# Optimization experiments

Hardware: AMD Instinct MI355X
Metric: run time of the kernel (lower is better)

## Reference

```python
import math
import jax, jax.numpy as jnp
import numpy as np

D = 1152      # vision_dim
P = 14        # patch
IMG = 896     # image_size
CIN = 3       # vision_channels
L = 2         # vision_blocks
MLP = 4304    # vision_mlp_hidden
EPS = 1e-6
B = 1
N = (IMG // P) ** 2  # 4096 tokens


def _ln(x, w, b):
    m = jnp.mean(x, axis=-1, keepdims=True)
    v = jnp.mean(jnp.square(x - m), axis=-1, keepdims=True)
    return (x - m) * jax.lax.rsqrt(v + EPS) * w + b


def setup_inputs() -> dict:
    key = jax.random.key(0)
    ks = jax.random.split(key, 20)
    s = 0.02
    inp = {
        "img": jax.random.normal(ks[0], (B, CIN, IMG, IMG), jnp.float32),
        "patch_w": jax.random.normal(ks[1], (D, CIN, P, P), jnp.float32) * s,
        "patch_b": jnp.zeros((D,), jnp.float32),
        "pos": jax.random.normal(ks[2], (D, N), jnp.float32) * s,
        # per-block params stacked along leading L axis (torch Linear: [out, in])
        "ln1_w": jnp.ones((L, D), jnp.float32),
        "ln1_b": jnp.zeros((L, D), jnp.float32),
        "qkv_w": jax.random.normal(ks[3], (L, 3 * D, D), jnp.float32) * s,
        "qkv_b": jnp.zeros((L, 3 * D), jnp.float32),
        "proj_w": jax.random.normal(ks[4], (L, D, D), jnp.float32) * s,
        "proj_b": jnp.zeros((L, D), jnp.float32),
        "ln2_w": jnp.ones((L, D), jnp.float32),
        "ln2_b": jnp.zeros((L, D), jnp.float32),
        "fc1_w": jax.random.normal(ks[5], (L, MLP, D), jnp.float32) * s,
        "fc1_b": jnp.zeros((L, MLP), jnp.float32),
        "fc2_w": jax.random.normal(ks[6], (L, D, MLP), jnp.float32) * s,
        "fc2_b": jnp.zeros((L, D), jnp.float32),
        "post_w": jnp.ones((D,), jnp.float32),
        "post_b": jnp.zeros((D,), jnp.float32),
    }
    return inp


def reference(img, patch_w, patch_b, pos, ln1_w, ln1_b, qkv_w, qkv_b,
              proj_w, proj_b, ln2_w, ln2_b, fc1_w, fc1_b, fc2_w, fc2_b,
              post_w, post_b):
    # conv patch embed (kernel=stride=P, valid padding)
    x = jax.lax.conv_general_dilated(
        img, patch_w, window_strides=(P, P), padding="VALID",
        dimension_numbers=("NCHW", "OIHW", "NCHW"))
    x = x + patch_b[None, :, None, None]
    x = x.reshape(B, D, N).transpose(0, 2, 1)          # [B, N, D]
    x = x + pos.T[None, :, :]

    scale = 1.0 / math.sqrt(D)

    def blk(x, p):
        l1w, l1b, qw, qb, pw, pb, l2w, l2b, f1w, f1b, f2w, f2b = p
        h = _ln(x, l1w, l1b)
        qkv = jnp.einsum("bnd,ed->bne", h, qw) + qb     # [B, N, 3D]
        q, k, v = jnp.split(qkv, 3, axis=-1)            # single-head, full D
        attn = jax.nn.softmax(jnp.einsum("bnd,bmd->bnm", q, k) * scale, axis=-1)
        y = jnp.einsum("bnm,bmd->bnd", attn, v)
        x = x + jnp.einsum("bnd,ed->bne", y, pw) + pb
        h = _ln(x, l2w, l2b)
        h = jax.nn.gelu(jnp.einsum("bnd,md->bnm", h, f1w) + f1b, approximate=False)
        x = x + jnp.einsum("bnm,dm->bnd", h, f2w) + f2b
        return x, None

    x, _ = jax.lax.scan(blk, x, (ln1_w, ln1_b, qkv_w, qkv_b, proj_w, proj_b,
                                 ln2_w, ln2_b, fc1_w, fc1_b, fc2_w, fc2_b))
    return _ln(x, post_w, post_b)
```

## Files before the change

### kernel.cpp

```cpp
#include <hip/hip_runtime.h>

#define NT 4096
#define DD 1152
#define D3 3456
#define MLP_R 4304
#define MLP_P 4352
#define KP 640

typedef unsigned short u16;
typedef short v8s __attribute__((ext_vector_type(8)));
typedef float v4f __attribute__((ext_vector_type(4)));

__device__ __forceinline__ u16 f2b(float f) {
    unsigned int u = __builtin_bit_cast(unsigned int, f);
    u += 0x7fffu + ((u >> 16) & 1u);
    return (u16)(u >> 16);
}
__device__ __forceinline__ float b2f(u16 s) {
    unsigned int u = ((unsigned int)s) << 16;
    return __builtin_bit_cast(float, u);
}

__device__ __forceinline__ void async16(const void* g, void* l) {
    __builtin_amdgcn_global_load_lds(
        (const __attribute__((address_space(1))) void*)g,
        (__attribute__((address_space(3))) void*)l, 16, 0, 0);
}

__device__ __forceinline__ unsigned lds_off(const void* p) {
    return (unsigned)(size_t)(const __attribute__((address_space(3))) void*)p;
}
__device__ __forceinline__ v8s ldsr(unsigned byte_off) {
    v8s r;
    asm volatile("ds_read_b128 %0, %1" : "=v"(r) : "v"(byte_off));
    return r;
}

__device__ __forceinline__ float gelu_f(float t) {
    float u = t * (0.7978845608028654f + 0.03567740814183026f * t * t);
    return t / (1.0f + __expf(-2.0f * u));
}

template<int EPI>
__global__ __launch_bounds__(512, 2)
void gemm8p(const u16* __restrict__ A, const u16* __restrict__ B, int ld,
            int Kdim, const float* __restrict__ bias,
            u16* __restrict__ outb, int ldc, int NNT)
{
    __shared__ __align__(128) union { u16 kl[2][32768]; u16 ep[8][8192]; } sm;
    const int tid  = threadIdx.x, lane = tid & 63, wave = tid >> 6;
    const int wr   = wave >> 2, wc = wave & 3;
    const int fr   = lane & 15, kqh = lane >> 4;

    const int nwg  = gridDim.x;
    const int bidx = (int)blockIdx.x;
    const int wg   = (bidx & 7) * (nwg >> 3) + (bidx >> 3);
    const int mt   = wg / NNT, nt = wg % NNT;
    const int bm0  = mt * 256, bn0 = nt * 256;

    const int c    = tid;
    const int s_lr = (c >> 7) * 16 + ((c >> 2) & 15);
    const int s_lc = ((((c >> 6) & 1) * 4) + ((c & 3) ^ (((c >> 5) & 1) << 1))) * 8;
    const size_t s_off = (size_t)s_lr * ld + s_lc;
    const unsigned koff2 = (unsigned)(fr * 64 + ((kqh * 16) ^ ((fr & 8) << 2)));

    u16* kb = sm.kl[0];
    const unsigned lbase = lds_off(kb);

    auto stage = [&](int bi, int reg, const u16* gRowBase) {
        u16* lb = kb + bi * 32768 + reg * 4096;
        async16(gRowBase + s_off, lb + tid * 8);
        async16(gRowBase + s_off + (size_t)64 * ld, lb + (512 + tid) * 8);
    };
    auto srcA = [&](int h, int t) { return A + (size_t)(bm0 + h * 128) * ld + t * 64; };
    auto srcB = [&](int h, int t) { return B + (size_t)(bn0 + h * 128) * ld + t * 64; };

    v4f acc[8][4];
    const v4f vzero = {0.f, 0.f, 0.f, 0.f};
#pragma unroll
    for (int i = 0; i < 8; ++i)
#pragma unroll
        for (int j = 0; j < 4; ++j) acc[i][j] = vzero;

    const int NKT = Kdim >> 6;

    stage(0, 4, srcB(0, 0));
    stage(0, 6, srcB(1, 0));
    stage(0, 0, srcA(0, 0));
    stage(0, 2, srcA(1, 0));
    if (NKT > 1) {
        stage(1, 4, srcB(0, 1));
        stage(1, 6, srcB(1, 1));
        asm volatile("s_waitcnt vmcnt(4)" ::: "memory");
    } else {
        asm volatile("s_waitcnt vmcnt(0)" ::: "memory");
    }
    __builtin_amdgcn_s_barrier();

    v8s a[8], b0f[4], b1f[4];
    for (int t = 0; t < NKT; ++t) {
        const int bi = t & 1;
        const unsigned AB = lbase + bi * 65536 + wr * 16384;
        const unsigned BB = lbase + bi * 65536 + 32768 + (wc >> 1) * 16384;
        const unsigned bs = (wc & 1) * 8192;

#pragma unroll
        for (int mi = 0; mi < 4; ++mi)
#pragma unroll
            for (int ks = 0; ks < 2; ++ks)
                a[mi * 2 + ks] = ldsr(AB + (mi * 2 + ks) * 1024 + koff2);
#pragma unroll
        for (int nj = 0; nj < 2; ++nj)
#pragma unroll
            for (int ks = 0; ks < 2; ++ks)
                b0f[nj * 2 + ks] = ldsr(BB + bs + (nj * 2 + ks) * 1024 + koff2);
        if (t + 1 < NKT) stage(bi ^ 1, 0, srcA(0, t + 1));
        __builtin_amdgcn_s_barrier();
        asm volatile("s_waitcnt lgkmcnt(0)" ::: "memory");
        __builtin_amdgcn_sched_barrier(0);
        __builtin_amdgcn_s_setprio(1);
#pragma unroll
        for (int mi = 0; mi < 4; ++mi)
#pragma unroll
            for (int nj = 0; nj < 2; ++nj)
#pragma unroll
                for (int ks = 0; ks < 2; ++ks)
                    acc[mi][nj] = __builtin_amdgcn_mfma_f32_16x16x32_bf16(
                        a[mi * 2 + ks], b0f[nj * 2 + ks], acc[mi][nj], 0, 0, 0);
        __builtin_amdgcn_s_setprio(0);
        __builtin_amdgcn_s_barrier();

#pragma unroll
        for (int nj = 0; nj < 2; ++nj)
#pragma unroll
            for (int ks = 0; ks < 2; ++ks)
                b1f[nj * 2 + ks] = ldsr(BB + bs + (4 + nj * 2 + ks) * 1024 + koff2);
        if (t + 1 < NKT) stage(bi ^ 1, 2, srcA(1, t + 1));
        __builtin_amdgcn_s_barrier();
        asm volatile("s_waitcnt lgkmcnt(0)" ::: "memory");
        __builtin_amdgcn_sched_barrier(0);
        __builtin_amdgcn_s_setprio(1);
#pragma unroll
        for (int mi = 0; mi < 4; ++mi)
#pragma unroll
            for (int nj = 0; nj < 2; ++nj)
#pragma unroll
                for (int ks = 0; ks < 2; ++ks)
                    acc[mi][2 + nj] = __builtin_amdgcn_mfma_f32_16x16x32_bf16(
                        a[mi * 2 + ks], b1f[nj * 2 + ks], acc[mi][2 + nj], 0, 0, 0);
        __builtin_amdgcn_s_setprio(0);
        __builtin_amdgcn_s_barrier();

#pragma unroll
        for (int mi = 0; mi < 4; ++mi)
#pragma unroll
            for (int ks = 0; ks < 2; ++ks)
                a[mi * 2 + ks] = ldsr(AB + (8 + mi * 2 + ks) * 1024 + koff2);
        if (t + 2 < NKT) stage(bi, 4, srcB(0, t + 2));
        __builtin_amdgcn_s_barrier();
        asm volatile("s_waitcnt lgkmcnt(0)" ::: "memory");
        __builtin_amdgcn_sched_barrier(0);
        __builtin_amdgcn_s_setprio(1);
#pragma unroll
        for (int mi = 0; mi < 4; ++mi)
#pragma unroll
            for (int nj = 0; nj < 2; ++nj)
#pragma unroll
                for (int ks = 0; ks < 2; ++ks)
                    acc[4 + mi][2 + nj] = __builtin_amdgcn_mfma_f32_16x16x32_bf16(
                        a[mi * 2 + ks], b1f[nj * 2 + ks], acc[4 + mi][2 + nj], 0, 0, 0);
        __builtin_amdgcn_s_setprio(0);
        __builtin_amdgcn_s_barrier();

        if (t + 2 < NKT) stage(bi, 6, srcB(1, t + 2));
        __builtin_amdgcn_s_barrier();
        __builtin_amdgcn_s_setprio(1);
#pragma unroll
        for (int mi = 0; mi < 4; ++mi)
#pragma unroll
            for (int nj = 0; nj < 2; ++nj)
#pragma unroll
                for (int ks = 0; ks < 2; ++ks)
                    acc[4 + mi][nj] = __builtin_amdgcn_mfma_f32_16x16x32_bf16(
                        a[mi * 2 + ks], b0f[nj * 2 + ks], acc[4 + mi][nj], 0, 0, 0);
        __builtin_amdgcn_s_setprio(0);
        asm volatile("s_waitcnt vmcnt(4)" ::: "memory");
        __builtin_amdgcn_s_barrier();
    }

    asm volatile("s_waitcnt vmcnt(0)" ::: "memory");
    __builtin_amdgcn_s_barrier();
    u16* ew = sm.ep[wave];
    float bcol[4];
    if constexpr (EPI >= 1) {
#pragma unroll
        for (int nj = 0; nj < 4; ++nj)
            bcol[nj] = bias[bn0 + wc * 64 + nj * 16 + fr];
    }
#pragma unroll
    for (int mi = 0; mi < 8; ++mi)
#pragma unroll
        for (int nj = 0; nj < 4; ++nj)
#pragma unroll
            for (int r = 0; r < 4; ++r) {
                int row = mi * 16 + kqh * 4 + r;
                int ec  = nj * 16 + fr;
                float t = acc[mi][nj][r];
                if constexpr (EPI >= 1) t += bcol[nj];
                if constexpr (EPI == 2) t = gelu_f(t);
                ew[row * 64 + (ec ^ (((row >> 2) & 3) << 4))] = f2b(t);
            }
    __syncthreads();
#pragma unroll
    for (int p = 0; p < 16; ++p) {
        int row = p * 8 + (lane >> 3);
        int key = (row >> 2) & 3;
        v8s ch = *(const v8s*)(ew + row * 64 + (((lane & 7) * 8) ^ (key << 4)));
        size_t gm = (size_t)(bm0 + wr * 128 + row);
        int gc = bn0 + wc * 64 + (lane & 7) * 8;
        *(uint4*)(outb + gm * ldc + gc) = __builtin_bit_cast(uint4, ch);
    }
}

template<int EPI, int MT, int DBUF = 0>
__global__ __launch_bounds__(256)
void gemm_bt(const u16* __restrict__ A, int lda,
             const u16* __restrict__ B, int ldb, int Kdim,
             const float* __restrict__ bias, const float* __restrict__ aux,
             float* __restrict__ outf, u16* __restrict__ outb, int ldc,
             u16* __restrict__ vt, int NX)
{
    constexpr int JT = (MT == 128) ? 4 : 2;
    constexpr int AR = MT * 8 / 256;
    constexpr int NB = DBUF ? 2 : 1;

    __shared__ union SM {
        struct { u16 a[NB * MT * 64]; u16 b[NB * 128 * 64]; } st;
        float sc[4][64][17];
    } sm;

    const int b    = blockIdx.x;
    const int MY   = (gridDim.x >> 3) / NX;
    const int q    = b >> 3;
    const int m0   = ((b & 7) * MY + q % MY) * MT;
    const int n0   = (q / MY) * 128;

    const int tid  = threadIdx.x;
    const int lane = tid & 63;
    const int wave = tid >> 6;
    const int wm   = (MT == 128) ? (wave & 1) * 64 : 0;
    const int wn   = (MT == 128) ? (wave >> 1) * 64 : wave * 32;
    const int fr   = lane & 15;
    const int kqh  = lane >> 4;
    const int swz  = fr & 7;

    v4f acc[4][JT];
    const v4f vzero = {0.f, 0.f, 0.f, 0.f};
#pragma unroll
    for (int i = 0; i < 4; ++i)
#pragma unroll
        for (int j = 0; j < JT; ++j) acc[i][j] = vzero;

    auto stage = [&](u16* As, u16* Bs, int kt) {
#pragma unroll
        for (int r = 0; r < AR; ++r) {
            int c = r * 256 + tid;
            int row = c >> 3;
            int kc = (c & 7) ^ (row & 7);
            async16(A + (size_t)(m0 + row) * lda + kt + kc * 8, As + c * 8);
        }
#pragma unroll
        for (int r = 0; r < 4; ++r) {
            int c = r * 256 + tid;
            int row = c >> 3;
            int kc = (c & 7) ^ (row & 7);
            async16(B + (size_t)(n0 + row) * ldb + kt + kc * 8, Bs + c * 8);
        }
    };

    auto compute = [&](const u16* As, const u16* Bs) {
#pragma unroll
        for (int ks = 0; ks < 2; ++ks) {
            const int kq = ks * 4 + kqh;
            const int kp = (kq ^ swz) * 8;
            v8s af[4], bf[JT];
#pragma unroll
            for (int i = 0; i < 4; ++i)
                af[i] = *(const v8s*)(As + (wm + i * 16 + fr) * 64 + kp);
#pragma unroll
            for (int j = 0; j < JT; ++j)
                bf[j] = *(const v8s*)(Bs + (wn + j * 16 + fr) * 64 + kp);
#pragma unroll
            for (int i = 0; i < 4; ++i)
#pragma unroll
                for (int j = 0; j < JT; ++j)
                    acc[i][j] = __builtin_amdgcn_mfma_f32_16x16x32_bf16(
                        af[i], bf[j], acc[i][j], 0, 0, 0);
        }
    };

    if constexpr (DBUF) {
        stage(sm.st.a, sm.st.b, 0);
        int cur = 0;
        for (int kt = 0; kt < Kdim; kt += 64) {
            __syncthreads();
            const int nxt = cur ^ 1;
            if (kt + 64 < Kdim)
                stage(sm.st.a + nxt * (MT * 64), sm.st.b + nxt * (128 * 64), kt + 64);
            compute(sm.st.a + cur * (MT * 64), sm.st.b + cur * (128 * 64));
            cur = nxt;
        }
    } else {
        for (int kt = 0; kt < Kdim; kt += 64) {
            stage(sm.st.a, sm.st.b, kt);
            __syncthreads();
            compute(sm.st.a, sm.st.b);
            __syncthreads();
        }
    }

    const int cn = lane & 15;
    const int cm = (lane >> 4) * 4;
    float (*S)[17] = sm.sc[wave];
    const int gm = m0 + wm + lane;
#pragma unroll
    for (int jp = 0; jp < JT; ++jp) {
        __syncthreads();
#pragma unroll
        for (int i = 0; i < 4; ++i)
#pragma unroll
            for (int r = 0; r < 4; ++r)
                S[i * 16 + cm + r][cn] = acc[i][jp][r];
        __syncthreads();
        const int gn0 = n0 + wn + jp * 16;
        float v[16];
#pragma unroll
        for (int c = 0; c < 16; ++c) v[c] = S[lane][c];
        if constexpr (EPI <= 2) {
            union { u16 us[16]; uint4 q4[2]; } o;
#pragma unroll
            for (int c = 0; c < 16; ++c) {
                float t = v[c];
                if constexpr (EPI >= 1) t += bias[gn0 + c];
                if constexpr (EPI == 2) t = gelu_f(t);
                o.us[c] = f2b(t);
            }
            uint4* dst = (uint4*)(outb + (size_t)gm * ldc + gn0);
            dst[0] = o.q4[0];
            dst[1] = o.q4[1];
            if constexpr (EPI == 1) {
                if (vt != nullptr && gn0 >= 2304) {
#pragma unroll
                    for (int c = 0; c < 16; ++c)
                        vt[(size_t)(gn0 + c - 2304) * NT + gm] = o.us[c];
                }
            }
        } else if constexpr (EPI == 3) {
            float* dst = outf + (size_t)gm * ldc + gn0;
            const float* ax = aux + (size_t)gm * ldc + gn0;
#pragma unroll
            for (int c = 0; c < 4; ++c) {
                float4 a4 = ((const float4*)ax)[c];
                float4 r4;
                r4.x = a4.x + v[4 * c + 0] + bias[gn0 + 4 * c + 0];
                r4.y = a4.y + v[4 * c + 1] + bias[gn0 + 4 * c + 1];
                r4.z = a4.z + v[4 * c + 2] + bias[gn0 + 4 * c + 2];
                r4.w = a4.w + v[4 * c + 3] + bias[gn0 + 4 * c + 3];
                ((float4*)dst)[c] = r4;
            }
        } else {
            float* dst = outf + (size_t)gm * ldc + gn0;
#pragma unroll
            for (int c = 0; c < 4; ++c) {
                float4 r4;
                r4.x = v[4 * c + 0] + bias[gn0 + 4 * c + 0] + aux[(size_t)(gn0 + 4 * c + 0) * NT + gm];
                r4.y = v[4 * c + 1] + bias[gn0 + 4 * c + 1] + aux[(size_t)(gn0 + 4 * c + 1) * NT + gm];
                r4.z = v[4 * c + 2] + bias[gn0 + 4 * c + 2] + aux[(size_t)(gn0 + 4 * c + 2) * NT + gm];
                r4.w = v[4 * c + 3] + bias[gn0 + 4 * c + 3] + aux[(size_t)(gn0 + 4 * c + 3) * NT + gm];
                ((float4*)dst)[c] = r4;
            }
        }
    }
}

template<int OUTF>
__global__ __launch_bounds__(384)
void ln_kernel(const float* __restrict__ x, const float* __restrict__ w,
               const float* __restrict__ b, void* __restrict__ out)
{
    const int n = blockIdx.x;
    const int t = threadIdx.x;
    const float* row = x + (size_t)n * DD;
    float v0 = row[t], v1 = row[t + 384], v2 = row[t + 768];
    float s  = v0 + v1 + v2;
    float ss = v0 * v0 + v1 * v1 + v2 * v2;
#pragma unroll
    for (int o = 32; o > 0; o >>= 1) {
        s  += __shfl_down(s, o);
        ss += __shfl_down(ss, o);
    }
    __shared__ float ps[6], pss[6], mh[2];
    if ((t & 63) == 0) { ps[t >> 6] = s; pss[t >> 6] = ss; }
    __syncthreads();
    if (t == 0) {
        float S = 0.f, SS = 0.f;
        for (int i = 0; i < 6; ++i) { S += ps[i]; SS += pss[i]; }
        float m = S / (float)DD;
        float var = SS / (float)DD - m * m;
        mh[0] = m;
        mh[1] = rsqrtf(var + 1e-6f);
    }
    __syncthreads();
    const float m = mh[0], rs = mh[1];
#pragma unroll
    for (int j = 0; j < 3; ++j) {
        int c = t + j * 384;
        float y = (row[c] - m) * rs * w[c] + b[c];
        if constexpr (OUTF) ((float*)out)[(size_t)n * DD + c] = y;
        else                ((u16*)out)[(size_t)n * DD + c]   = f2b(y);
    }
}

__global__ __launch_bounds__(256)
void softmax_kernel(u16* __restrict__ s)
{
    const float SC = 0.029462782549439484f;
    const int row = blockIdx.x;
    const int t = threadIdx.x;
    u16* p = s + (size_t)row * NT + t * 16;
    uint4 u0 = *(const uint4*)p;
    uint4 u1 = *(const uint4*)(p + 8);
    float v[16];
    unsigned int w[8] = {u0.x, u0.y, u0.z, u0.w, u1.x, u1.y, u1.z, u1.w};
#pragma unroll
    for (int i = 0; i < 8; ++i) {
        v[2 * i]     = b2f((u16)(w[i] & 0xffffu)) * SC;
        v[2 * i + 1] = b2f((u16)(w[i] >> 16)) * SC;
    }
    float mx = -1e30f;
#pragma unroll
    for (int i = 0; i < 16; ++i) mx = fmaxf(mx, v[i]);
#pragma unroll
    for (int o = 32; o > 0; o >>= 1) mx = fmaxf(mx, __shfl_down(mx, o));
    __shared__ float red[4];
    __shared__ float bc;
    if ((t & 63) == 0) red[t >> 6] = mx;
    __syncthreads();
    if (t == 0) bc = fmaxf(fmaxf(red[0], red[1]), fmaxf(red[2], red[3]));
    __syncthreads();
    const float M = bc;
    float sum = 0.f;
#pragma unroll
    for (int i = 0; i < 16; ++i) { v[i] = __expf(v[i] - M); sum += v[i]; }
#pragma unroll
    for (int o = 32; o > 0; o >>= 1) sum += __shfl_down(sum, o);
    __syncthreads();
    if ((t & 63) == 0) red[t >> 6] = sum;
    __syncthreads();
    if (t == 0) bc = red[0] + red[1] + red[2] + red[3];
    __syncthreads();
    const float inv = 1.0f / bc;
    union { u16 us[8]; uint4 u4; } o0, o1;
#pragma unroll
    for (int i = 0; i < 8; ++i) o0.us[i] = f2b(v[i] * inv);
#pragma unroll
    for (int i = 0; i < 8; ++i) o1.us[i] = f2b(v[8 + i] * inv);
    *(uint4*)p = o0.u4;
    *(uint4*)(p + 8) = o1.u4;
}

__global__ __launch_bounds__(256)
void im2col_kernel(const float* __restrict__ img, u16* __restrict__ a)
{
    const int k = blockIdx.x * 256 + threadIdx.x;
    const int n = blockIdx.y;
    if (k >= KP) return;
    float v = 0.f;
    if (k < 588) {
        int cin = k / 196;
        int rr = k - cin * 196;
        int py = rr / 14;
        int px = rr - py * 14;
        int gy = (n >> 6) * 14 + py;
        int gx = (n & 63) * 14 + px;
        v = img[(size_t)cin * 896 * 896 + (size_t)gy * 896 + gx];
    }
    a[(size_t)n * KP + k] = f2b(v);
}

constexpr int CV_S0 = 2 * D3 * DD / 4;
constexpr int CV_S1 = CV_S0 + 2 * DD * DD / 4;
constexpr int CV_S2 = CV_S1 + 2 * MLP_P * DD / 4;
constexpr int CV_S3 = CV_S2 + 2 * DD * MLP_P / 4;
constexpr int CV_S4 = CV_S3 + DD * KP / 4;
constexpr int CV_S5 = CV_S4 + 2 * MLP_P / 4;
constexpr int CV_BLOCKS = (CV_S5 + 255) / 256;

__device__ __forceinline__ void store_bf4(u16* p, float4 f) {
    union { u16 s[4]; uint2 d; } o;
    o.s[0] = f2b(f.x); o.s[1] = f2b(f.y); o.s[2] = f2b(f.z); o.s[3] = f2b(f.w);
    *(uint2*)p = o.d;
}

__global__ __launch_bounds__(256)
void convert_all(const float* __restrict__ qkv_w, const float* __restrict__ proj_w,
                 const float* __restrict__ fc1_w, const float* __restrict__ fc2_w,
                 const float* __restrict__ patch_w, const float* __restrict__ fc1_b,
                 u16* __restrict__ w_qkv, u16* __restrict__ w_proj,
                 u16* __restrict__ w_fc1, u16* __restrict__ w_fc2,
                 u16* __restrict__ w_pat, float* __restrict__ fc1b_p)
{
    int v = blockIdx.x * 256 + threadIdx.x;
    if (v >= CV_S5) return;
    const float4 z4 = {0.f, 0.f, 0.f, 0.f};
    if (v < CV_S0) {
        store_bf4(w_qkv + (size_t)v * 4, ((const float4*)qkv_w)[v]);
    } else if (v < CV_S1) {
        int e = v - CV_S0;
        store_bf4(w_proj + (size_t)e * 4, ((const float4*)proj_w)[e]);
    } else if (v < CV_S2) {
        size_t e = (size_t)(v - CV_S1) * 4;
        int row = (int)(e / DD);
        int c = (int)(e % DD);
        int l = row / MLP_P, lr = row % MLP_P;
        float4 f = z4;
        if (lr < MLP_R)
            f = *(const float4*)(fc1_w + ((size_t)l * MLP_R + lr) * DD + c);
        store_bf4(w_fc1 + e, f);
    } else if (v < CV_S3) {
        size_t e = (size_t)(v - CV_S2) * 4;
        int row = (int)(e / MLP_P);
        int c = (int)(e % MLP_P);
        float4 f = z4;
        if (c < MLP_R)
            f = *(const float4*)(fc2_w + (size_t)row * MLP_R + c);
        store_bf4(w_fc2 + e, f);
    } else if (v < CV_S4) {
        size_t e = (size_t)(v - CV_S3) * 4;
        int row = (int)(e / KP);
        int c = (int)(e % KP);
        float4 f = z4;
        if (c < 588)
            f = *(const float4*)(patch_w + (size_t)row * 588 + c);
        store_bf4(w_pat + e, f);
    } else {
        size_t e = (size_t)(v - CV_S4) * 4;
        int l = (int)(e / MLP_P);
        int c = (int)(e % MLP_P);
        float4 f = z4;
        if (c < MLP_R)
            f = *(const float4*)(fc1_b + (size_t)l * MLP_R + c);
        *(float4*)(fc1b_p + e) = f;
    }
}

constexpr size_t OFF_X      = 0;
constexpr size_t OFF_HBF    = OFF_X      + (size_t)NT * DD * 4;
constexpr size_t OFF_TMP    = OFF_HBF    + (size_t)NT * DD * 2;
constexpr size_t OFF_QKV    = OFF_TMP    + (size_t)NT * MLP_P * 2;
constexpr size_t OFF_VT     = OFF_QKV    + (size_t)NT * D3 * 2;
constexpr size_t OFF_IM     = OFF_VT     + (size_t)DD * NT * 2;
constexpr size_t OFF_WQKV   = OFF_IM     + (size_t)NT * KP * 2;
constexpr size_t OFF_WPROJ  = OFF_WQKV   + (size_t)2 * D3 * DD * 2;
constexpr size_t OFF_WFC1   = OFF_WPROJ  + (size_t)2 * DD * DD * 2;
constexpr size_t OFF_WFC2   = OFF_WFC1   + (size_t)2 * MLP_P * DD * 2;
constexpr size_t OFF_WPATCH = OFF_WFC2   + (size_t)2 * DD * MLP_P * 2;
constexpr size_t OFF_FC1B   = OFF_WPATCH + (size_t)DD * KP * 2;

extern "C" void kernel_launch(void* const* d_in, const int* in_sizes, int n_in,
                              void* d_out, int out_size, void* d_ws, size_t ws_size,
                              hipStream_t stream)
{
    const float* img     = (const float*)d_in[0];
    const float* patch_w = (const float*)d_in[1];
    const float* patch_b = (const float*)d_in[2];
    const float* pos     = (const float*)d_in[3];
    const float* ln1_w   = (const float*)d_in[4];
    const float* ln1_b   = (const float*)d_in[5];
    const float* qkv_w   = (const float*)d_in[6];
    const float* qkv_b   = (const float*)d_in[7];
    const float* proj_w  = (const float*)d_in[8];
    const float* proj_b  = (const float*)d_in[9];
    const float* ln2_w   = (const float*)d_in[10];
    const float* ln2_b   = (const float*)d_in[11];
    const float* fc1_w   = (const float*)d_in[12];
    const float* fc1_b   = (const float*)d_in[13];
    const float* fc2_w   = (const float*)d_in[14];
    const float* fc2_b   = (const float*)d_in[15];
    const float* post_w  = (const float*)d_in[16];
    const float* post_b  = (const float*)d_in[17];

    char* ws = (char*)d_ws;
    float* x      = (float*)(ws + OFF_X);
    u16*  h_bf    = (u16*)(ws + OFF_HBF);
    u16*  tmp_bf  = (u16*)(ws + OFF_TMP);
    u16*  qkv_bf  = (u16*)(ws + OFF_QKV);
    u16*  vt      = (u16*)(ws + OFF_VT);
    u16*  a_im    = (u16*)(ws + OFF_IM);
    u16*  w_qkv   = (u16*)(ws + OFF_WQKV);
    u16*  w_proj  = (u16*)(ws + OFF_WPROJ);
    u16*  w_fc1   = (u16*)(ws + OFF_WFC1);
    u16*  w_fc2   = (u16*)(ws + OFF_WFC2);
    u16*  w_pat   = (u16*)(ws + OFF_WPATCH);
    float* fc1b_p = (float*)(ws + OFF_FC1B);

    convert_all<<<CV_BLOCKS, 256, 0, stream>>>(
        qkv_w, proj_w, fc1_w, fc2_w, patch_w, fc1_b,
        w_qkv, w_proj, w_fc1, w_fc2, w_pat, fc1b_p);
    im2col_kernel<<<dim3(3, NT), 256, 0, stream>>>(img, a_im);

    gemm_bt<4, 64, 1><<<9 * 64, 256, 0, stream>>>(
        a_im, KP, w_pat, KP, KP, patch_b, pos, x, nullptr, DD, nullptr, 9);

    for (int l = 0; l < 2; ++l) {
        ln_kernel<0><<<NT, 384, 0, stream>>>(x, ln1_w + l * DD, ln1_b + l * DD, h_bf);
        gemm_bt<1, 128><<<27 * 32, 256, 0, stream>>>(
            h_bf, DD, w_qkv + (size_t)l * D3 * DD, DD, DD,
            qkv_b + (size_t)l * D3, nullptr, nullptr, qkv_bf, D3, vt, 27);
        gemm8p<0><<<256, 512, 0, stream>>>(
            qkv_bf, qkv_bf + DD, D3, DD, nullptr, tmp_bf, NT, 16);
        softmax_kernel<<<NT, 256, 0, stream>>>(tmp_bf);
        gemm_bt<0, 64, 1><<<9 * 64, 256, 0, stream>>>(
            tmp_bf, NT, vt, NT, NT, nullptr, nullptr, nullptr, h_bf, DD, nullptr, 9);
        gemm_bt<3, 64, 1><<<9 * 64, 256, 0, stream>>>(
            h_bf, DD, w_proj + (size_t)l * DD * DD, DD, DD,
            proj_b + (size_t)l * DD, x, x, nullptr, DD, nullptr, 9);
        ln_kernel<0><<<NT, 384, 0, stream>>>(x, ln2_w + l * DD, ln2_b + l * DD, h_bf);
        gemm8p<2><<<272, 512, 0, stream>>>(
            h_bf, w_fc1 + (size_t)l * MLP_P * DD, DD, DD,
            fc1b_p + (size_t)l * MLP_P, tmp_bf, MLP_P, 17);
        gemm_bt<3, 64, 1><<<9 * 64, 256, 0, stream>>>(
            tmp_bf, MLP_P, w_fc2 + (size_t)l * DD * MLP_P, MLP_P, MLP_P,
            fc2_b + (size_t)l * DD, x, x, nullptr, DD, nullptr, 9);
    }
    ln_kernel<1><<<NT, 384, 0, stream>>>(x, post_w, post_b, d_out);
}
```

Before: 912.0 us.

## Prefetch next B fragments and overlap LDS reads with MFMA via partial waits

Restructures the GEMM main loop so the first B fragment set for the next K tile is read from LDS at the end of the current iteration, and the current A and second-half B fragments are loaded up front. The full lgkmcnt(0) waits are replaced by staged lgkmcnt(n) waits, so each group of MFMAs can start as soon as its own A fragments arrive. This hides LDS read latency behind matrix math instead of stalling all MFMAs on every read. It changes the order in which accumulator quadrants are computed and relies on exact in-order lgkmcnt counting, which adds correctness risk around the wait counts and the final-iteration vmcnt handling.

Result: no change. 925.0 us (+1.4%).

```diff
diff --git a/kernel.cpp b/kernel.cpp
--- a/kernel.cpp
+++ b/kernel.cpp
@@ -35,6 +35,9 @@
     asm volatile("ds_read_b128 %0, %1" : "=v"(r) : "v"(byte_off));
     return r;
 }
+
+#define LGKM_SB(n) do { asm volatile("s_waitcnt lgkmcnt(" #n ")" ::: "memory"); \
+                        __builtin_amdgcn_sched_barrier(0); } while (0)
 
 __device__ __forceinline__ float gelu_f(float t) {
     float u = t * (0.7978845608028654f + 0.03567740814183026f * t * t);
@@ -66,6 +69,9 @@
 
     u16* kb = sm.kl[0];
     const unsigned lbase = lds_off(kb);
+    const unsigned bs    = (wc & 1) * 8192;
+    const unsigned ABc   = lbase + wr * 16384;
+    const unsigned BBc   = lbase + 32768 + (wc >> 1) * 16384 + bs;
 
     auto stage = [&](int bi, int reg, const u16* gRowBase) {
         u16* lb = kb + bi * 32768 + reg * 4096;
@@ -81,6 +87,16 @@
     for (int i = 0; i < 8; ++i)
 #pragma unroll
         for (int j = 0; j < 4; ++j) acc[i][j] = vzero;
+
+    v8s a[8], b01[4], b23[4];
+    auto mfma4 = [&](int r, int cb, const v8s* bv, int g) {
+#pragma unroll
+        for (int nj = 0; nj < 2; ++nj)
+#pragma unroll
+            for (int ks = 0; ks < 2; ++ks)
+                acc[r][cb + nj] = __builtin_amdgcn_mfma_f32_16x16x32_bf16(
+                    a[g * 2 + ks], bv[nj * 2 + ks], acc[r][cb + nj], 0, 0, 0);
+    };
 
     const int NKT = Kdim >> 6;
 
@@ -96,95 +112,63 @@
         asm volatile("s_waitcnt vmcnt(0)" ::: "memory");
     }
     __builtin_amdgcn_s_barrier();
-
-    v8s a[8], b0f[4], b1f[4];
+#pragma unroll
+    for (int q = 0; q < 4; ++q) b01[q] = ldsr(BBc + q * 1024 + koff2);
+
     for (int t = 0; t < NKT; ++t) {
         const int bi = t & 1;
-        const unsigned AB = lbase + bi * 65536 + wr * 16384;
-        const unsigned BB = lbase + bi * 65536 + 32768 + (wc >> 1) * 16384;
-        const unsigned bs = (wc & 1) * 8192;
-
-#pragma unroll
-        for (int mi = 0; mi < 4; ++mi)
-#pragma unroll
-            for (int ks = 0; ks < 2; ++ks)
-                a[mi * 2 + ks] = ldsr(AB + (mi * 2 + ks) * 1024 + koff2);
-#pragma unroll
-        for (int nj = 0; nj < 2; ++nj)
-#pragma unroll
-            for (int ks = 0; ks < 2; ++ks)
-                b0f[nj * 2 + ks] = ldsr(BB + bs + (nj * 2 + ks) * 1024 + koff2);
+        const unsigned AB  = ABc + bi * 65536;
+        const unsigned BB  = BBc + bi * 65536;
+        const unsigned BBn = BBc + (bi ^ 1) * 65536;
+
+#pragma unroll
+        for (int q = 0; q < 8; ++q) a[q] = ldsr(AB + q * 1024 + koff2);
+#pragma unroll
+        for (int q = 0; q < 4; ++q) b23[q] = ldsr(BB + (4 + q) * 1024 + koff2);
         if (t + 1 < NKT) stage(bi ^ 1, 0, srcA(0, t + 1));
         __builtin_amdgcn_s_barrier();
-        asm volatile("s_waitcnt lgkmcnt(0)" ::: "memory");
+        __builtin_amdgcn_s_setprio(1);
+        LGKM_SB(10); mfma4(0, 0, b01, 0); __builtin_amdgcn_sched_barrier(0);
+        LGKM_SB(8);  mfma4(1, 0, b01, 1); __builtin_amdgcn_sched_barrier(0);
+        LGKM_SB(6);  mfma4(2, 0, b01, 2); __builtin_amdgcn_sched_barrier(0);
+        LGKM_SB(4);  mfma4(3, 0, b01, 3);
+        __builtin_amdgcn_s_setprio(0);
+        __builtin_amdgcn_s_barrier();
+
+        if (t + 1 < NKT) stage(bi ^ 1, 2, srcA(1, t + 1));
+        __builtin_amdgcn_s_barrier();
+        __builtin_amdgcn_s_setprio(1);
+        LGKM_SB(0);
+#pragma unroll
+        for (int mi = 0; mi < 4; ++mi) mfma4(mi, 2, b23, mi);
+        __builtin_amdgcn_s_setprio(0);
+        __builtin_amdgcn_s_barrier();
+
+#pragma unroll
+        for (int q = 0; q < 8; ++q) a[q] = ldsr(AB + (8 + q) * 1024 + koff2);
+        if (t + 2 < NKT) stage(bi, 4, srcB(0, t + 2));
+        __builtin_amdgcn_s_barrier();
+        __builtin_amdgcn_s_setprio(1);
+        LGKM_SB(6); mfma4(4, 0, b01, 0); __builtin_amdgcn_sched_barrier(0);
+        LGKM_SB(4); mfma4(5, 0, b01, 1); __builtin_amdgcn_sched_barrier(0);
+        LGKM_SB(2); mfma4(6, 0, b01, 2); __builtin_amdgcn_sched_barrier(0);
+        LGKM_SB(0); mfma4(7, 0, b01, 3);
+        __builtin_amdgcn_s_setprio(0);
+        __builtin_amdgcn_s_barrier();
+
+        if (t + 2 < NKT) stage(bi, 6, srcB(1, t + 2));
+        if (t + 2 < NKT) { asm volatile("s_waitcnt vmcnt(4)" ::: "memory"); }
+        else             { asm volatile("s_waitcnt vmcnt(0)" ::: "memory"); }
+        __builtin_amdgcn_s_barrier();
+        if (t + 1 < NKT) {
+#pragma unroll
+            for (int q = 0; q < 4; ++q) b01[q] = ldsr(BBn + q * 1024 + koff2);
+        }
         __builtin_amdgcn_sched_barrier(0);
         __builtin_amdgcn_s_setprio(1);
 #pragma unroll
-        for (int mi = 0; mi < 4; ++mi)
-#pragma unroll
-            for (int nj = 0; nj < 2; ++nj)
-#pragma unroll
-                for (int ks = 0; ks < 2; ++ks)
-                    acc[mi][nj] = __builtin_amdgcn_mfma_f32_16x16x32_bf16(
-                        a[mi * 2 + ks], b0f[nj * 2 + ks], acc[mi][nj], 0, 0, 0);
+        for (int mi = 0; mi < 4; ++mi) mfma4(4 + mi, 2, b23, mi);
         __builtin_amdgcn_s_setprio(0);
-        __builtin_amdgcn_s_barrier();
-
-#pragma unroll
-        for (int nj = 0; nj < 2; ++nj)
-#pragma unroll
-            for (int ks = 0; ks < 2; ++ks)
-                b1f[nj * 2 + ks] = ldsr(BB + bs + (4 + nj * 2 + ks) * 1024 + koff2);
-        if (t + 1 < NKT) stage(bi ^ 1, 2, srcA(1, t + 1));
-        __builtin_amdgcn_s_barrier();
-        asm volatile("s_waitcnt lgkmcnt(0)" ::: "memory");
-        __builtin_amdgcn_sched_barrier(0);
-        __builtin_amdgcn_s_setprio(1);
-#pragma unroll
-        for (int mi = 0; mi < 4; ++mi)
-#pragma unroll
-            for (int nj = 0; nj < 2; ++nj)
-#pragma unroll
-                for (int ks = 0; ks < 2; ++ks)
-                    acc[mi][2 + nj] = __builtin_amdgcn_mfma_f32_16x16x32_bf16(
-                        a[mi * 2 + ks], b1f[nj * 2 + ks], acc[mi][2 + nj], 0, 0, 0);
-        __builtin_amdgcn_s_setprio(0);
-        __builtin_amdgcn_s_barrier();
-
-#pragma unroll
-        for (int mi = 0; mi < 4; ++mi)
-#pragma unroll
-            for (int ks = 0; ks < 2; ++ks)
-                a[mi * 2 + ks] = ldsr(AB + (8 + mi * 2 + ks) * 1024 + koff2);
-        if (t + 2 < NKT) stage(bi, 4, srcB(0, t + 2));
-        __builtin_amdgcn_s_barrier();
-        asm volatile("s_waitcnt lgkmcnt(0)" ::: "memory");
-        __builtin_amdgcn_sched_barrier(0);
-        __builtin_amdgcn_s_setprio(1);
-#pragma unroll
-        for (int mi = 0; mi < 4; ++mi)
-#pragma unroll
-            for (int nj = 0; nj < 2; ++nj)
-#pragma unroll
-                for (int ks = 0; ks < 2; ++ks)
-                    acc[4 + mi][2 + nj] = __builtin_amdgcn_mfma_f32_16x16x32_bf16(
-                        a[mi * 2 + ks], b1f[nj * 2 + ks], acc[4 + mi][2 + nj], 0, 0, 0);
-        __builtin_amdgcn_s_setprio(0);
-        __builtin_amdgcn_s_barrier();
-
-        if (t + 2 < NKT) stage(bi, 6, srcB(1, t + 2));
-        __builtin_amdgcn_s_barrier();
-        __builtin_amdgcn_s_setprio(1);
-#pragma unroll
-        for (int mi = 0; mi < 4; ++mi)
-#pragma unroll
-            for (int nj = 0; nj < 2; ++nj)
-#pragma unroll
-                for (int ks = 0; ks < 2; ++ks)
-                    acc[4 + mi][nj] = __builtin_amdgcn_mfma_f32_16x16x32_bf16(
-                        a[mi * 2 + ks], b0f[nj * 2 + ks], acc[4 + mi][nj], 0, 0, 0);
-        __builtin_amdgcn_s_setprio(0);
-        asm volatile("s_waitcnt vmcnt(4)" ::: "memory");
         __builtin_amdgcn_s_barrier();
     }
 
```

## Run QKV projection on 256x256 gemm8p kernel with padded weights and fused V transpose

Applied to the files above, without the earlier changes.

Moves the QKV projection from the 128-tile gemm_bt kernel to the larger 256x256 eight-wave gemm8p kernel. To make this fit, the QKV weights and bias are padded to 3584 columns during conversion, and the qkv buffer stride changes to match. The epilogue also writes the transposed V slice as scattered 2-byte stores. The pipeline tail now waits for all loads to finish. In exchange it computes an extra padded column tile, and the transposed V writes are uncoalesced.

New measurement: 913.9 us. No clear change (+0.2%).

```diff
diff --git a/kernel.cpp b/kernel.cpp
--- a/kernel.cpp
+++ b/kernel.cpp
@@ -3,6 +3,7 @@
 #define NT 4096
 #define DD 1152
 #define D3 3456
+#define D3P 3584
 #define MLP_R 4304
 #define MLP_P 4352
 #define KP 640
@@ -45,7 +46,7 @@
 __global__ __launch_bounds__(512, 2)
 void gemm8p(const u16* __restrict__ A, const u16* __restrict__ B, int ld,
             int Kdim, const float* __restrict__ bias,
-            u16* __restrict__ outb, int ldc, int NNT)
+            u16* __restrict__ outb, int ldc, int NNT, u16* __restrict__ vt)
 {
     __shared__ __align__(128) union { u16 kl[2][32768]; u16 ep[8][8192]; } sm;
     const int tid  = threadIdx.x, lane = tid & 63, wave = tid >> 6;
@@ -184,7 +185,8 @@
                     acc[4 + mi][nj] = __builtin_amdgcn_mfma_f32_16x16x32_bf16(
                         a[mi * 2 + ks], b0f[nj * 2 + ks], acc[4 + mi][nj], 0, 0, 0);
         __builtin_amdgcn_s_setprio(0);
-        asm volatile("s_waitcnt vmcnt(4)" ::: "memory");
+        if (t + 2 < NKT) { asm volatile("s_waitcnt vmcnt(4)" ::: "memory"); }
+        else             { asm volatile("s_waitcnt vmcnt(0)" ::: "memory"); }
         __builtin_amdgcn_s_barrier();
     }
 
@@ -211,14 +213,23 @@
                 ew[row * 64 + (ec ^ (((row >> 2) & 3) << 4))] = f2b(t);
             }
     __syncthreads();
+    const int gc = bn0 + wc * 64 + (lane & 7) * 8;
+    const bool inV = (EPI == 1) && (vt != nullptr) && gc >= 2304 && gc < D3;
 #pragma unroll
     for (int p = 0; p < 16; ++p) {
         int row = p * 8 + (lane >> 3);
         int key = (row >> 2) & 3;
         v8s ch = *(const v8s*)(ew + row * 64 + (((lane & 7) * 8) ^ (key << 4)));
         size_t gm = (size_t)(bm0 + wr * 128 + row);
-        int gc = bn0 + wc * 64 + (lane & 7) * 8;
         *(uint4*)(outb + gm * ldc + gc) = __builtin_bit_cast(uint4, ch);
+        if constexpr (EPI == 1) {
+            if (inV) {
+                union { v8s v; u16 us[8]; } cu; cu.v = ch;
+#pragma unroll
+                for (int j = 0; j < 8; ++j)
+                    vt[(size_t)(gc + j - 2304) * NT + gm] = cu.us[j];
+            }
+        }
     }
 }
 
@@ -488,13 +499,14 @@
     a[(size_t)n * KP + k] = f2b(v);
 }
 
-constexpr int CV_S0 = 2 * D3 * DD / 4;
+constexpr int CV_S0 = 2 * D3P * DD / 4;
 constexpr int CV_S1 = CV_S0 + 2 * DD * DD / 4;
 constexpr int CV_S2 = CV_S1 + 2 * MLP_P * DD / 4;
 constexpr int CV_S3 = CV_S2 + 2 * DD * MLP_P / 4;
 constexpr int CV_S4 = CV_S3 + DD * KP / 4;
 constexpr int CV_S5 = CV_S4 + 2 * MLP_P / 4;
-constexpr int CV_BLOCKS = (CV_S5 + 255) / 256;
+constexpr int CV_S6 = CV_S5 + 2 * D3P / 4;
+constexpr int CV_BLOCKS = (CV_S6 + 255) / 256;
 
 __device__ __forceinline__ void store_bf4(u16* p, float4 f) {
     union { u16 s[4]; uint2 d; } o;
@@ -506,15 +518,24 @@
 void convert_all(const float* __restrict__ qkv_w, const float* __restrict__ proj_w,
                  const float* __restrict__ fc1_w, const float* __restrict__ fc2_w,
                  const float* __restrict__ patch_w, const float* __restrict__ fc1_b,
+                 const float* __restrict__ qkv_b,
                  u16* __restrict__ w_qkv, u16* __restrict__ w_proj,
                  u16* __restrict__ w_fc1, u16* __restrict__ w_fc2,
-                 u16* __restrict__ w_pat, float* __restrict__ fc1b_p)
+                 u16* __restrict__ w_pat, float* __restrict__ fc1b_p,
+                 float* __restrict__ qkvb_p)
 {
     int v = blockIdx.x * 256 + threadIdx.x;
-    if (v >= CV_S5) return;
+    if (v >= CV_S6) return;
     const float4 z4 = {0.f, 0.f, 0.f, 0.f};
     if (v < CV_S0) {
-        store_bf4(w_qkv + (size_t)v * 4, ((const float4*)qkv_w)[v]);
+        size_t e = (size_t)v * 4;
+        int row = (int)(e / DD);
+        int c = (int)(e % DD);
+        int l = row / D3P, lr = row % D3P;
+        float4 f = z4;
+        if (lr < D3)
+            f = *(const float4*)(qkv_w + ((size_t)l * D3 + lr) * DD + c);
+        store_bf4(w_qkv + e, f);
     } else if (v < CV_S1) {
         int e = v - CV_S0;
         store_bf4(w_proj + (size_t)e * 4, ((const float4*)proj_w)[e]);
@@ -543,7 +564,7 @@
         if (c < 588)
             f = *(const float4*)(patch_w + (size_t)row * 588 + c);
         store_bf4(w_pat + e, f);
-    } else {
+    } else if (v < CV_S5) {
         size_t e = (size_t)(v - CV_S4) * 4;
         int l = (int)(e / MLP_P);
         int c = (int)(e % MLP_P);
@@ -551,6 +572,14 @@
         if (c < MLP_R)
             f = *(const float4*)(fc1_b + (size_t)l * MLP_R + c);
         *(float4*)(fc1b_p + e) = f;
+    } else {
+        size_t e = (size_t)(v - CV_S5) * 4;
+        int l = (int)(e / D3P);
+        int c = (int)(e % D3P);
+        float4 f = z4;
+        if (c < D3)
+            f = *(const float4*)(qkv_b + (size_t)l * D3 + c);
+        *(float4*)(qkvb_p + e) = f;
     }
 }
 
@@ -558,14 +587,15 @@
 constexpr size_t OFF_HBF    = OFF_X      + (size_t)NT * DD * 4;
 constexpr size_t OFF_TMP    = OFF_HBF    + (size_t)NT * DD * 2;
 constexpr size_t OFF_QKV    = OFF_TMP    + (size_t)NT * MLP_P * 2;
-constexpr size_t OFF_VT     = OFF_QKV    + (size_t)NT * D3 * 2;
+constexpr size_t OFF_VT     = OFF_QKV    + (size_t)NT * D3P * 2;
 constexpr size_t OFF_IM     = OFF_VT     + (size_t)DD * NT * 2;
 constexpr size_t OFF_WQKV   = OFF_IM     + (size_t)NT * KP * 2;
-constexpr size_t OFF_WPROJ  = OFF_WQKV   + (size_t)2 * D3 * DD * 2;
+constexpr size_t OFF_WPROJ  = OFF_WQKV   + (size_t)2 * D3P * DD * 2;
 constexpr size_t OFF_WFC1   = OFF_WPROJ  + (size_t)2 * DD * DD * 2;
 constexpr size_t OFF_WFC2   = OFF_WFC1   + (size_t)2 * MLP_P * DD * 2;
 constexpr size_t OFF_WPATCH = OFF_WFC2   + (size_t)2 * DD * MLP_P * 2;
 constexpr size_t OFF_FC1B   = OFF_WPATCH + (size_t)DD * KP * 2;
+constexpr size_t OFF_QKVB   = OFF_FC1B   + (size_t)2 * MLP_P * 4;
 
 extern "C" void kernel_launch(void* const* d_in, const int* in_sizes, int n_in,
                               void* d_out, int out_size, void* d_ws, size_t ws_size,
@@ -603,10 +633,11 @@
     u16*  w_fc2   = (u16*)(ws + OFF_WFC2);
     u16*  w_pat   = (u16*)(ws + OFF_WPATCH);
     float* fc1b_p = (float*)(ws + OFF_FC1B);
+    float* qkvb_p = (float*)(ws + OFF_QKVB);
 
     convert_all<<<CV_BLOCKS, 256, 0, stream>>>(
-        qkv_w, proj_w, fc1_w, fc2_w, patch_w, fc1_b,
-        w_qkv, w_proj, w_fc1, w_fc2, w_pat, fc1b_p);
+        qkv_w, proj_w, fc1_w, fc2_w, patch_w, fc1_b, qkv_b,
+        w_qkv, w_proj, w_fc1, w_fc2, w_pat, fc1b_p, qkvb_p);
     im2col_kernel<<<dim3(3, NT), 256, 0, stream>>>(img, a_im);
 
     gemm_bt<4, 64, 1><<<9 * 64, 256, 0, stream>>>(
@@ -614,11 +645,11 @@
 
     for (int l = 0; l < 2; ++l) {
         ln_kernel<0><<<NT, 384, 0, stream>>>(x, ln1_w + l * DD, ln1_b + l * DD, h_bf);
-        gemm_bt<1, 128><<<27 * 32, 256, 0, stream>>>(
-            h_bf, DD, w_qkv + (size_t)l * D3 * DD, DD, DD,
-            qkv_b + (size_t)l * D3, nullptr, nullptr, qkv_bf, D3, vt, 27);
+        gemm8p<1><<<224, 512, 0, stream>>>(
+            h_bf, w_qkv + (size_t)l * D3P * DD, DD, DD,
+            qkvb_p + (size_t)l * D3P, qkv_bf, D3P, 14, vt);
         gemm8p<0><<<256, 512, 0, stream>>>(
-            qkv_bf, qkv_bf + DD, D3, DD, nullptr, tmp_bf, NT, 16);
+            qkv_bf, qkv_bf + DD, D3P, DD, nullptr, tmp_bf, NT, 16, nullptr);
         softmax_kernel<<<NT, 256, 0, stream>>>(tmp_bf);
         gemm_bt<0, 64, 1><<<9 * 64, 256, 0, stream>>>(
             tmp_bf, NT, vt, NT, NT, nullptr, nullptr, nullptr, h_bf, DD, nullptr, 9);
@@ -628,7 +659,7 @@
         ln_kernel<0><<<NT, 384, 0, stream>>>(x, ln2_w + l * DD, ln2_b + l * DD, h_bf);
         gemm8p<2><<<272, 512, 0, stream>>>(
             h_bf, w_fc1 + (size_t)l * MLP_P * DD, DD, DD,
-            fc1b_p + (size_t)l * MLP_P, tmp_bf, MLP_P, 17);
+            fc1b_p + (size_t)l * MLP_P, tmp_bf, MLP_P, 17, nullptr);
         gemm_bt<3, 64, 1><<<9 * 64, 256, 0, stream>>>(
             tmp_bf, MLP_P, w_fc2 + (size_t)l * DD * MLP_P, MLP_P, MLP_P,
             fc2_b + (size_t)l * DD, x, x, nullptr, DD, nullptr, 9);
```
